# Optimization experiments

Hardware: AMD Instinct MI355X
Metric: run time of the kernel (lower is better)

Reference implementation:

```python
import jax, jax.numpy as jnp
import numpy as np

V, D, F, H, NB, S, B = 16384, 512, 2048, 8, 4, 512, 2
T_STEPS = 3      # config.T: number of PC inference iterations
GAMMA = 0.1      # state-update step size


def _layernorm(x, s, b):
    m = x.mean(-1, keepdims=True)
    v = ((x - m) ** 2).mean(-1, keepdims=True)
    return (x - m) * jax.lax.rsqrt(v + 1e-5) * s + b


def setup_inputs() -> dict:
    key = jax.random.key(0)
    ks = jax.random.split(key, 12)
    r = lambda k, sh: jax.random.normal(k, sh, jnp.float32) * 0.02
    return {
        'word_emb': r(ks[0], (V, D)),
        'pos_emb': r(ks[1], (S, D)),
        'Wq': r(ks[2], (NB, D, D)),
        'Wk': r(ks[3], (NB, D, D)),
        'Wv': r(ks[4], (NB, D, D)),
        'bq': jnp.zeros((NB, D), jnp.float32),
        'bk': jnp.zeros((NB, D), jnp.float32),
        'bv': jnp.zeros((NB, D), jnp.float32),
        'Wo': r(ks[5], (NB, D, D)),
        'bo': jnp.zeros((NB, D), jnp.float32),
        'ln1_s': jnp.ones((NB, D), jnp.float32),
        'ln1_b': jnp.zeros((NB, D), jnp.float32),
        'ln2_s': jnp.ones((NB, D), jnp.float32),
        'ln2_b': jnp.zeros((NB, D), jnp.float32),
        'W1': r(ks[6], (NB, D, F)),
        'b1': jnp.zeros((NB, F), jnp.float32),
        'W2': r(ks[7], (NB, F, D)),
        'b2': jnp.zeros((NB, D), jnp.float32),
        'Wout': r(ks[8], (D, V)),
        'bout': jnp.zeros((V,), jnp.float32),
        'input_ids': jax.random.randint(ks[9], (B, S), 0, V),
        'target_ids': jax.random.randint(ks[10], (B, S), 0, V),
    }


def _forward(word_emb, pos_emb, Wq, Wk, Wv, bq, bk, bv, Wo, bo,
             ln1_s, ln1_b, ln2_s, ln2_b, W1, b1, W2, b2, Wout, bout,
             input_ids, target_ids):
    Bsz, Sl = input_ids.shape
    dh = D // H
    scale = 1.0 / float(np.sqrt(dh))
    ids = jnp.clip(input_ids, 0, V - 1)
    target = jax.nn.one_hot(jnp.clip(target_ids, 0, V - 1), V, dtype=word_emb.dtype)
    # bottom prediction: word + position embeddings
    mu_emb = word_emb[ids] + pos_emb[jnp.arange(Sl)][None]  # (B,S,D)
    causal = jnp.tril(jnp.ones((Sl, Sl), bool))
    neg = jnp.finfo(word_emb.dtype).min

    def attn(x, b):
        h = _layernorm(x, ln1_s[b], ln1_b[b])
        q = (h @ Wq[b] + bq[b]).reshape(Bsz, Sl, H, dh)
        k = (h @ Wk[b] + bk[b]).reshape(Bsz, Sl, H, dh)
        v = (h @ Wv[b] + bv[b]).reshape(Bsz, Sl, H, dh)
        sc = jnp.einsum('bqhd,bkhd->bhqk', q, k) * scale
        sc = jnp.where(causal, sc, neg)
        a = jax.nn.softmax(sc, axis=-1)
        return jnp.einsum('bhqk,bkhd->bqhd', a, v).reshape(Bsz, Sl, D)

    # generative functions g[l]: x_l -> mu_{l+1}; 4 PC layers per block
    # (pc_qkv->attn ctx, pc_output->Wo, pc_layer1->gelu(fc1), pc_layer2->fc2)
    gs = []
    for b in range(NB):
        gs.append(lambda x, b=b: attn(x, b))
        gs.append(lambda x, b=b: x @ Wo[b] + bo[b])
        gs.append(lambda x, b=b: jax.nn.gelu(_layernorm(x, ln2_s[b], ln2_b[b]) @ W1[b] + b1[b]))
        gs.append(lambda x, b=b: x @ W2[b] + b2[b])
    g_top = lambda x: x @ Wout + bout  # output pc layer -> logits mu

    # init_x: forward sweep sets each latent to its prediction
    xs = [mu_emb]
    for g in gs:
        xs.append(g(xs[-1]))
    L = len(gs)

    # T-step iterative PC inference: eps_l = x_l - mu_l, top clamped to target
    # x_l <- x_l + GAMMA * (J_{g_l}(x_l)^T eps_{l+1} - eps_l)
    for _ in range(T_STEPS):
        preds, vjps = [], []
        for l in range(L):
            mu, vj = jax.vjp(gs[l], xs[l])
            preds.append(mu)
            vjps.append(vj)
        logits, vj_top = jax.vjp(g_top, xs[L])
        eps = [xs[0] - mu_emb] + [xs[l + 1] - preds[l] for l in range(L)]
        eps_top = logits - target
        new_xs = []
        for l in range(L + 1):
            td = vjps[l](eps[l + 1])[0] if l < L else vj_top(eps_top)[0]
            new_xs.append(xs[l] + GAMMA * (td - eps[l]))
        xs = new_xs

    return g_top(xs[L])  # get_mu('linear_output')


def reference(word_emb, pos_emb, Wq, Wk, Wv, bq, bk, bv, Wo, bo,
              ln1_s, ln1_b, ln2_s, ln2_b, W1, b1, W2, b2, Wout, bout,
              input_ids, target_ids):
    return _forward(word_emb, pos_emb, Wq, Wk, Wv, bq, bk, bv, Wo, bo,
                    ln1_s, ln1_b, ln2_s, ln2_b, W1, b1, W2, b2, Wout, bout,
                    input_ids, target_ids)
```

## Files before the change

### kernel.cpp

```cpp
#include <hip/hip_runtime.h>
#include <hip/hip_bf16.h>
#include <math.h>

#define D_   512
#define F_   2048
#define V_   16384
#define H_   8
#define DH_  64
#define S_   512
#define B_   2
#define M_   1024
#define MD_  (M_ * D_)
#define MF_  (M_ * F_)
#define GAMMA_ 0.1f

typedef unsigned int u32;
typedef unsigned short u16;
typedef __attribute__((ext_vector_type(4))) float f32x4;
typedef __attribute__((ext_vector_type(8))) short s16x8;
typedef __attribute__((ext_vector_type(4))) u16 u16x4;
typedef __attribute__((ext_vector_type(8))) u16 u16x8;

__device__ __forceinline__ u16 f2b(float f) {
    __hip_bfloat16 h = __float2bfloat16(f);
    return *reinterpret_cast<u16*>(&h);
}
__device__ __forceinline__ u16x4 pack4(f32x4 v) {
    u16x4 o; o.x = f2b(v[0]); o.y = f2b(v[1]); o.z = f2b(v[2]); o.w = f2b(v[3]);
    return o;
}

__device__ __forceinline__ void gl_lds16(const void* g, void* l) {
    __builtin_amdgcn_global_load_lds((const __attribute__((address_space(1))) u32*)g,
                                     (__attribute__((address_space(3))) u32*)l, 16, 0, 0);
}

__device__ __forceinline__ float gelu_f(float v) {
    float u = 0.7978845608028654f * (v + 0.044715f * v * v * v);
    return 0.5f * v * (1.f + tanhf(u));
}

__device__ __forceinline__ f32x4 xpose4(f32x4 v, int b) {
#pragma unroll
    for (int s = 1; s < 4; s <<= 1) {
        f32x4 nv;
#pragma unroll
        for (int j = 0; j < 4; ++j) {
            float ex = __shfl_xor(v[j ^ s], s, 64);
            nv[j] = ((b ^ j) & s) ? ex : v[j];
        }
        v = nv;
    }
    return v;
}

__device__ __forceinline__ float blk_sum(float v, float* sh) {
#pragma unroll
    for (int o = 32; o > 0; o >>= 1) v += __shfl_down(v, o, 64);
    int lane = threadIdx.x & 63, w = threadIdx.x >> 6;
    if (lane == 0) sh[w] = v;
    __syncthreads();
    float r = sh[0] + sh[1] + sh[2] + sh[3];
    __syncthreads();
    return r;
}

__device__ __forceinline__ float wave_sum(float v) {
#pragma unroll
    for (int o = 32; o > 0; o >>= 1) v += __shfl_xor(v, o, 64);
    return v;
}

#define E_F32   0
#define E_GELU  1
#define E_TD    2
#define E_X15B  3
#define E_EC    4
#define E_QKV3  5
#define E_OUT   6

template<int BK>
__device__ __forceinline__ int swz(int c, int row) {
    if constexpr (BK == 32) return c ^ ((row >> 1) & 3);
    else                    return c ^ (row & 7);
}

template<int BM, int BN, int BK, int FM, int FN, int EPI>
__global__ __launch_bounds__(256)
void mfma_gemm(const u16* __restrict__ A, const u16* __restrict__ B,
               float* __restrict__ Cf, u16* __restrict__ Cb,
               u16* __restrict__ Cb2, u16* __restrict__ Cb3,
               const float* __restrict__ bias,
               int K, int lda, int ldb, int ldc,
               long sC, long sKz, float alpha,
               const float* __restrict__ base, const float* __restrict__ subv,
               const float* __restrict__ cvec, const float* __restrict__ woutF,
               const int* __restrict__ tcl,
               float* __restrict__ ebF, u16* __restrict__ ebB)
{
    constexpr int WC = BN / (FN * 16);
    static_assert((BM / (FM * 16)) * WC == 4, "4 waves");
    constexpr int LPR = BK / 8;
    constexpr int RPI = 2048 / BK;
    __shared__ __align__(16) u16 Asl[2][BM * BK];
    __shared__ __align__(16) u16 Bsl[2][BN * BK];
    const int t = threadIdx.x, l = t & 63, wid = t >> 6;
    const int m0 = blockIdx.y * BM, n0 = blockIdx.x * BN;
    const long z = blockIdx.z;
    A += z * sKz;
    B += z * sKz;
    if (Cf) Cf += z * sC;

    f32x4 acc[FM][FN] = {};
    const int rm = (wid / WC) * (FM * 16), cn = (wid % WC) * (FN * 16);
    const int lr = l & 15, hi = l >> 4;
    const int srl = t / LPR, sc = t % LPR;

    auto stage = [&](int k0, int pb) {
#pragma unroll
        for (int i = 0; i < BM / RPI; ++i) {
            int row = i * RPI + srl;
            gl_lds16(A + (size_t)(m0 + row) * lda + k0 + swz<BK>(sc, row) * 8,
                     &Asl[pb][i * 2048 + t * 8]);
        }
#pragma unroll
        for (int i = 0; i < BN / RPI; ++i) {
            int row = i * RPI + srl;
            gl_lds16(B + (size_t)(n0 + row) * ldb + k0 + swz<BK>(sc, row) * 8,
                     &Bsl[pb][i * 2048 + t * 8]);
        }
    };
    auto compute = [&](int pb) {
#pragma unroll
        for (int kk = 0; kk < BK / 32; ++kk) {
            s16x8 av[FM], bv[FN];
#pragma unroll
            for (int fm = 0; fm < FM; ++fm)
                av[fm] = *(const s16x8*)&Asl[pb][(rm + fm * 16 + lr) * BK + swz<BK>(kk * 4 + hi, lr) * 8];
#pragma unroll
            for (int fn = 0; fn < FN; ++fn)
                bv[fn] = *(const s16x8*)&Bsl[pb][(cn + fn * 16 + lr) * BK + swz<BK>(kk * 4 + hi, lr) * 8];
#pragma unroll
            for (int fm = 0; fm < FM; ++fm)
#pragma unroll
                for (int fn = 0; fn < FN; ++fn)
                    acc[fm][fn] = __builtin_amdgcn_mfma_f32_16x16x32_bf16(av[fm], bv[fn], acc[fm][fn], 0, 0, 0);
        }
    };

    stage(0, 0);
    __syncthreads();
    int cur = 0;
    for (int k0 = BK; k0 < K; k0 += BK) {
        stage(k0, cur ^ 1);
        compute(cur);
        __syncthreads();
        cur ^= 1;
    }
    compute(cur);

    const int qb = lr & 3, qi = lr >> 2;
#pragma unroll
    for (int fm = 0; fm < FM; ++fm)
#pragma unroll
        for (int fn = 0; fn < FN; ++fn) {
            const int gm = m0 + rm + fm * 16 + hi * 4 + qb;
            const int gn0 = n0 + cn + fn * 16 + qi * 4;
            const size_t idx0 = (size_t)gm * ldc + gn0;
            if constexpr (EPI == E_QKV3) {
                const int gnf = n0 + cn + fn * 16;
                const int sel = gnf >> 9;
                if (sel < 2) {
                    f32x4 v = xpose4(acc[fm][fn], qb);
                    f32x4 bv4 = *(const f32x4*)&bias[gn0];
#pragma unroll
                    for (int j = 0; j < 4; ++j) v[j] += bv4[j];
                    int b = gm >> 9, s = gm & (S_ - 1);
                    int d9 = gn0 & 511, h = d9 >> 6, d = d9 & 63;
                    u16* dst = (sel == 0) ? Cb : Cb2;
                    *(u16x4*)&dst[(((size_t)(b * H_ + h) * S_ + s) << 6) + d] = pack4(v);
                } else {
                    const int gnl = gnf + lr;
                    const int gm0 = m0 + rm + fm * 16 + hi * 4;
                    int b = gm0 >> 9, s0 = gm0 & (S_ - 1);
                    int d9 = gnl & 511, h = d9 >> 6, d = d9 & 63;
                    float bb = bias[gnl];
                    f32x4 v = acc[fm][fn];
#pragma unroll
                    for (int j = 0; j < 4; ++j) v[j] += bb;
                    *(u16x4*)&Cb3[((((size_t)(b * H_ + h)) << 6) + d) * S_ + s0] = pack4(v);
                }
            } else {
                f32x4 v = xpose4(acc[fm][fn], qb);
                if constexpr (EPI == E_F32) {
#pragma unroll
                    for (int j = 0; j < 4; ++j) v[j] *= alpha;
                    if (bias) {
                        f32x4 bv4 = *(const f32x4*)&bias[gn0];
#pragma unroll
                        for (int j = 0; j < 4; ++j) v[j] += bv4[j];
                    }
                    *(f32x4*)&Cf[idx0] = v;
                    if (Cb) *(u16x4*)&Cb[idx0] = pack4(v);
                } else if constexpr (EPI == E_OUT) {
                    f32x4 bv4 = *(const f32x4*)&bias[gn0];
#pragma unroll
                    for (int j = 0; j < 4; ++j) v[j] += bv4[j];
                    *(f32x4*)&Cf[idx0] = v;
                } else if constexpr (EPI == E_GELU) {
                    f32x4 bv4 = *(const f32x4*)&bias[gn0];
#pragma unroll
                    for (int j = 0; j < 4; ++j) v[j] = gelu_f(v[j] + bv4[j]);
                    if (Cf) *(f32x4*)&Cf[idx0] = v;
                    *(u16x4*)&Cb[idx0] = pack4(v);
                } else if constexpr (EPI == E_TD) {
                    const int tc = tcl[gm];
                    f32x4 cv4 = *(const f32x4*)&cvec[gn0];
                    f32x4 ba4 = *(const f32x4*)&base[idx0];
                    f32x4 dlt, o2;
#pragma unroll
                    for (int j = 0; j < 4; ++j) {
                        float d = v[j] + cv4[j] - woutF[(size_t)(gn0 + j) * V_ + tc];
                        dlt[j] = GAMMA_ * d;
                    }
                    if (subv) {
                        f32x4 sv4 = *(const f32x4*)&subv[idx0];
#pragma unroll
                        for (int j = 0; j < 4; ++j) dlt[j] -= GAMMA_ * sv4[j];
                    }
#pragma unroll
                    for (int j = 0; j < 4; ++j) o2[j] = ba4[j] + dlt[j];
                    if (Cf) *(f32x4*)&Cf[idx0] = o2;
                    *(u16x4*)&Cb[idx0] = pack4(o2);
                    if (ebF) *(f32x4*)&ebF[idx0] = dlt;
                    if (ebB) *(u16x4*)&ebB[idx0] = pack4(dlt);
                } else if constexpr (EPI == E_X15B) {
                    f32x4 ba4 = *(const f32x4*)&base[idx0];
#pragma unroll
                    for (int j = 0; j < 4; ++j) v[j] = ba4[j] + GAMMA_ * v[j];
                    *(u16x4*)&Cb[idx0] = pack4(v);
                } else if constexpr (EPI == E_EC) {
                    f32x4 ba4 = *(const f32x4*)&base[idx0];
                    f32x4 bv4 = *(const f32x4*)&bias[gn0];
#pragma unroll
                    for (int j = 0; j < 4; ++j) v[j] = ba4[j] - (v[j] + bv4[j]);
                    *(f32x4*)&Cf[idx0] = v;
                }
            }
        }
}

__global__ __launch_bounds__(256)
void flash_attn(const u16* __restrict__ q, const u16* __restrict__ k,
                const u16* __restrict__ vT, u16* __restrict__ ctx)
{
    __shared__ __align__(16) u16 Ks[2][64 * 64];
    __shared__ __align__(16) u16 Vs[2][64 * 64];
    __shared__ __align__(16) u16 Ps[4][16 * 64];
    const int t = threadIdx.x, l = t & 63, w = t >> 6;
    const int qt = blockIdx.x, z = blockIdx.y;
    const int bb = z >> 3, hh = z & 7;
    const int lr = l & 15, hi = l >> 4;
    const u16* qp = q + (((size_t)z * S_ + qt * 64 + w * 16) << 6);
    const u16* kp = k + ((size_t)z * S_ << 6);
    const u16* vp = vT + (((size_t)z) << 6) * S_;

    const s16x8 aq0 = *(const s16x8*)&qp[lr * 64 + hi * 8];
    const s16x8 aq1 = *(const s16x8*)&qp[lr * 64 + 32 + hi * 8];

    f32x4 o[4] = {};
    float m[4], ls[4];
#pragma unroll
    for (int r = 0; r < 4; ++r) { m[r] = -3.0e38f; ls[r] = 0.f; }
    const int qrow = qt * 64 + w * 16 + hi * 4;
    const int srow = t >> 3, scl = t & 7;
    const int cg1 = (scl ^ (srow & 7)) * 8;
    const int srow2 = srow + 32;
    const int cg2 = (scl ^ (srow2 & 7)) * 8;
    const int sw7 = (lr & 7);

    auto stage = [&](int j, int pb) {
        gl_lds16(kp + ((size_t)(j * 64 + srow) << 6) + cg1, &Ks[pb][t * 8]);
        gl_lds16(vp + (size_t)srow * S_ + j * 64 + cg1, &Vs[pb][t * 8]);
        gl_lds16(kp + ((size_t)(j * 64 + srow2) << 6) + cg2, &Ks[pb][(t + 256) * 8]);
        gl_lds16(vp + (size_t)srow2 * S_ + j * 64 + cg2, &Vs[pb][(t + 256) * 8]);
    };

    stage(0, 0);
    __syncthreads();
    int cur = 0;
    for (int j = 0; j <= qt; ++j) {
        if (j < qt) stage(j + 1, cur ^ 1);

        float pv[4][4];
#pragma unroll
        for (int fn = 0; fn < 4; ++fn) {
            f32x4 acc = {};
            acc = __builtin_amdgcn_mfma_f32_16x16x32_bf16(aq0,
                    *(const s16x8*)&Ks[cur][((fn * 16 + lr) << 6) + ((hi ^ sw7) * 8)], acc, 0, 0, 0);
            acc = __builtin_amdgcn_mfma_f32_16x16x32_bf16(aq1,
                    *(const s16x8*)&Ks[cur][((fn * 16 + lr) << 6) + (((hi + 4) ^ sw7) * 8)], acc, 0, 0, 0);
#pragma unroll
            for (int r = 0; r < 4; ++r) pv[fn][r] = acc[r] * 0.125f;
        }
        if (j == qt) {
#pragma unroll
            for (int fn = 0; fn < 4; ++fn) {
                int col = j * 64 + fn * 16 + lr;
#pragma unroll
                for (int r = 0; r < 4; ++r)
                    if (col > qrow + r) pv[fn][r] = -3.0e38f;
            }
        }
        float sc[4], rs[4];
#pragma unroll
        for (int r = 0; r < 4; ++r) {
            float x = fmaxf(fmaxf(pv[0][r], pv[1][r]), fmaxf(pv[2][r], pv[3][r]));
#pragma unroll
            for (int off = 1; off < 16; off <<= 1) x = fmaxf(x, __shfl_xor(x, off, 64));
            float nm = fmaxf(m[r], x);
            sc[r] = expf(m[r] - nm);
            m[r] = nm;
            rs[r] = 0.f;
        }
#pragma unroll
        for (int fn = 0; fn < 4; ++fn)
#pragma unroll
            for (int r = 0; r < 4; ++r) {
                float p = expf(pv[fn][r] - m[r]);
                pv[fn][r] = p;
                rs[r] += p;
            }
#pragma unroll
        for (int r = 0; r < 4; ++r) {
#pragma unroll
            for (int off = 1; off < 16; off <<= 1) rs[r] += __shfl_xor(rs[r], off, 64);
            ls[r] = ls[r] * sc[r] + rs[r];
        }
#pragma unroll
        for (int fn = 0; fn < 4; ++fn)
#pragma unroll
            for (int r = 0; r < 4; ++r) o[fn][r] *= sc[r];
#pragma unroll
        for (int fn = 0; fn < 4; ++fn)
#pragma unroll
            for (int r = 0; r < 4; ++r) {
                int qr = hi * 4 + r;
                int ci = (2 * fn + (lr >> 3)) ^ (qr & 7);
                Ps[w][qr * 64 + ci * 8 + (lr & 7)] = f2b(pv[fn][r]);
            }
#pragma unroll
        for (int ks = 0; ks < 2; ++ks) {
            const s16x8 pa = *(const s16x8*)&Ps[w][lr * 64 + (((4 * ks + hi) ^ sw7) * 8)];
#pragma unroll
            for (int fn = 0; fn < 4; ++fn)
                o[fn] = __builtin_amdgcn_mfma_f32_16x16x32_bf16(pa,
                        *(const s16x8*)&Vs[cur][((fn * 16 + lr) << 6) + (((hi + 4 * ks) ^ sw7) * 8)], o[fn], 0, 0, 0);
        }
        __syncthreads();
        cur ^= 1;
    }
    float inv[4];
#pragma unroll
    for (int r = 0; r < 4; ++r) inv[r] = 1.f / ls[r];
    u16* cp = ctx + ((size_t)(bb * S_ + qt * 64 + w * 16) * D_) + hh * 64;
    const int qb = lr & 3, qi = lr >> 2;
#pragma unroll
    for (int fn = 0; fn < 4; ++fn) {
        f32x4 v = o[fn];
#pragma unroll
        for (int r = 0; r < 4; ++r) v[r] *= inv[r];
        v = xpose4(v, qb);
        *(u16x4*)&cp[(size_t)(hi * 4 + qb) * D_ + fn * 16 + qi * 4] = pack4(v);
    }
}

__global__ __launch_bounds__(256)
void mega_prep(const float* __restrict__ Wq, const float* __restrict__ Wk,
               const float* __restrict__ Wv, const float* __restrict__ Wo,
               const float* __restrict__ W1, const float* __restrict__ W2,
               const float* __restrict__ Wout,
               const float* __restrict__ bq, const float* __restrict__ bk,
               const float* __restrict__ bv, const int* __restrict__ target_ids,
               u16* __restrict__ wqkvT, u16* __restrict__ woT, u16* __restrict__ w1T,
               u16* __restrict__ w2T, u16* __restrict__ w2d, u16* __restrict__ woutT,
               u16* __restrict__ woutD, float* __restrict__ qkvb, int* __restrict__ tcl)
{
    __shared__ float tile[64][65];
    const int g = blockIdx.x, t = threadIdx.x;

    const float* in = nullptr;
    u16 *outT = nullptr, *outC = nullptr;
    int R = 512, C = 512, tx = 0, ty = 0;

    if (g < 768) {
        int sel = g / 256, rem = g % 256, zz = rem >> 6, tl = rem & 63;
        in = (sel == 0 ? Wq : sel == 1 ? Wk : Wv) + (size_t)zz * 262144;
        outT = wqkvT + (size_t)zz * 786432 + sel * 262144;
        tx = tl & 7; ty = tl >> 3;
    } else if (g < 1024) {
        int rem = g - 768, zz = rem >> 6, tl = rem & 63;
        in = Wo + (size_t)zz * 262144; outT = woT + (size_t)zz * 262144;
        tx = tl & 7; ty = tl >> 3;
    } else if (g < 2048) {
        int rem = g - 1024, zz = rem >> 8, tl = rem & 255;
        in = W1 + (size_t)zz * 1048576; outT = w1T + (size_t)zz * 1048576;
        C = 2048; tx = tl & 31; ty = tl >> 5;
    } else if (g < 3072) {
        int rem = g - 2048, zz = rem >> 8, tl = rem & 255;
        in = W2 + (size_t)zz * 1048576; outT = w2T + (size_t)zz * 1048576;
        if (zz == 3) outC = w2d;
        R = 2048; tx = tl & 7; ty = tl >> 3;
    } else if (g < 5120) {
        int tl = g - 3072;
        in = Wout; outT = woutT; outC = woutD;
        C = 16384; tx = tl & 255; ty = tl >> 8;
    } else {
        for (int i = t; i < M_; i += 256) {
            int v = target_ids[i];
            tcl[i] = v < 0 ? 0 : (v > V_ - 1 ? V_ - 1 : v);
        }
        for (int i = t; i < 4 * 1536; i += 256) {
            int b = i / 1536, j = i - b * 1536;
            qkvb[i] = (j < 512) ? bq[b * 512 + j]
                    : (j < 1024) ? bk[b * 512 + j - 512] : bv[b * 512 + j - 1024];
        }
        return;
    }

    const int r0 = ty * 64, c0 = tx * 64;
#pragma unroll
    for (int p = 0; p < 4; ++p) {
        int row = p * 16 + (t >> 4), col = (t & 15) * 4;
        float4 v = *(const float4*)&in[(size_t)(r0 + row) * C + c0 + col];
        tile[row][col] = v.x; tile[row][col + 1] = v.y;
        tile[row][col + 2] = v.z; tile[row][col + 3] = v.w;
        if (outC) {
            f32x4 fv; fv[0] = v.x; fv[1] = v.y; fv[2] = v.z; fv[3] = v.w;
            *(u16x4*)&outC[(size_t)(r0 + row) * C + c0 + col] = pack4(fv);
        }
    }
    __syncthreads();
#pragma unroll
    for (int p = 0; p < 2; ++p) {
        int orow = p * 32 + (t >> 3), oc = (t & 7) * 8;
        u16x8 o;
#pragma unroll
        for (int j = 0; j < 8; ++j) o[j] = f2b(tile[oc + j][orow]);
        *(u16x8*)&outT[(size_t)(c0 + orow) * R + r0 + oc] = o;
    }
}

__global__ __launch_bounds__(256)
void cvec_kernel(const float* __restrict__ Wout, const float* __restrict__ bout,
                 float* __restrict__ c)
{
    __shared__ float sh[4];
    int d = blockIdx.x;
    const float* row = Wout + (size_t)d * V_;
    float s = 0.f;
    for (int v = threadIdx.x * 4; v < V_; v += 1024) {
        float4 a = *(const float4*)&row[v];
        float4 b = *(const float4*)&bout[v];
        s += a.x * b.x + a.y * b.y + a.z * b.z + a.w * b.w;
    }
    float r = blk_sum(s, sh);
    if (threadIdx.x == 0) c[d] = r;
}

__global__ void gred_kernel(const float* __restrict__ P, u16* __restrict__ G)
{
    int i = blockIdx.x * blockDim.x + threadIdx.x;
    if (i < D_ * D_) {
        float s = 0.f;
#pragma unroll
        for (int zz = 0; zz < 16; ++zz) s += P[(size_t)zz * D_ * D_ + i];
        G[i] = f2b(s);
    }
}

__global__ void embed_kernel(const float4* __restrict__ we, const float4* __restrict__ pe,
                             const int* __restrict__ ids, float4* __restrict__ o)
{
    int t = blockIdx.x * blockDim.x + threadIdx.x;
    int d4 = t & 127, row = t >> 7;
    int ss = row & (S_ - 1);
    int id = ids[row];
    id = id < 0 ? 0 : (id > V_ - 1 ? V_ - 1 : id);
    float4 a = we[(size_t)id * 128 + d4];
    float4 b = pe[(size_t)ss * 128 + d4];
    o[(size_t)row * 128 + d4] = make_float4(a.x + b.x, a.y + b.y, a.z + b.z, a.w + b.w);
}

__global__ __launch_bounds__(256)
void ln_fwd_kernel(const float* __restrict__ x, const float* __restrict__ s,
                   const float* __restrict__ bb, u16* __restrict__ h)
{
    const int l = threadIdx.x & 63, w = threadIdx.x >> 6;
    const int row = blockIdx.x * 4 + w;
    const float* xr = x + (size_t)row * D_;
    const int c0 = l * 8;
    float4 a = *(const float4*)&xr[c0];
    float4 b = *(const float4*)&xr[c0 + 4];
    float sum = a.x + a.y + a.z + a.w + b.x + b.y + b.z + b.w;
    float mu = wave_sum(sum) * (1.f / D_);
    float d0 = a.x - mu, d1 = a.y - mu, d2 = a.z - mu, d3 = a.w - mu;
    float d4 = b.x - mu, d5 = b.y - mu, d6 = b.z - mu, d7 = b.w - mu;
    float vs = d0*d0 + d1*d1 + d2*d2 + d3*d3 + d4*d4 + d5*d5 + d6*d6 + d7*d7;
    float var = wave_sum(vs) * (1.f / D_);
    float r = rsqrtf(var + 1e-5f);
    float4 s0 = *(const float4*)&s[c0], s1 = *(const float4*)&s[c0 + 4];
    float4 b0 = *(const float4*)&bb[c0], b1 = *(const float4*)&bb[c0 + 4];
    u16* hr = h + (size_t)row * D_;
    f32x4 o0, o1;
    o0[0] = d0 * r * s0.x + b0.x; o0[1] = d1 * r * s0.y + b0.y;
    o0[2] = d2 * r * s0.z + b0.z; o0[3] = d3 * r * s0.w + b0.w;
    o1[0] = d4 * r * s1.x + b1.x; o1[1] = d5 * r * s1.y + b1.y;
    o1[2] = d6 * r * s1.z + b1.z; o1[3] = d7 * r * s1.w + b1.w;
    *(u16x4*)&hr[c0] = pack4(o0);
    *(u16x4*)&hr[c0 + 4] = pack4(o1);
}

extern "C" void kernel_launch(void* const* d_in, const int* in_sizes, int n_in,
                              void* d_out, int out_size, void* d_ws, size_t ws_size,
                              hipStream_t stream)
{
    (void)in_sizes; (void)n_in; (void)out_size;
    const float* Wq  = (const float*)d_in[2];
    const float* Wk  = (const float*)d_in[3];
    const float* Wv  = (const float*)d_in[4];
    const float* bq  = (const float*)d_in[5];
    const float* bk  = (const float*)d_in[6];
    const float* bv  = (const float*)d_in[7];
    const float* Wo  = (const float*)d_in[8];
    const float* bo  = (const float*)d_in[9];
    const float* ln1_s = (const float*)d_in[10];
    const float* ln1_b = (const float*)d_in[11];
    const float* ln2_s = (const float*)d_in[12];
    const float* ln2_b = (const float*)d_in[13];
    const float* W1  = (const float*)d_in[14];
    const float* b1  = (const float*)d_in[15];
    const float* W2  = (const float*)d_in[16];
    const float* b2  = (const float*)d_in[17];
    const float* Wout = (const float*)d_in[18];
    const float* bout = (const float*)d_in[19];
    const int* input_ids  = (const int*)d_in[20];
    const int* target_ids = (const int*)d_in[21];
    float* out = (float*)d_out;

    char* wsb = (char*)d_ws;
    size_t off = 0;
    auto alloc = [&](size_t bytes) -> void* {
        off = (off + 255) & ~(size_t)255;
        void* p = wsb + off; off += bytes; return p;
    };
    u16* wqkvT = (u16*)alloc((size_t)4 * 1536 * D_ * 2);
    u16* woT   = (u16*)alloc((size_t)4 * D_ * D_ * 2);
    u16* w1T   = (u16*)alloc((size_t)4 * D_ * F_ * 2);
    u16* w2T   = (u16*)alloc((size_t)4 * D_ * F_ * 2);
    u16* w2d   = (u16*)alloc((size_t)F_ * D_ * 2);
    u16* woutT = (u16*)alloc((size_t)V_ * D_ * 2);
    u16* G_b   = (u16*)alloc((size_t)D_ * D_ * 2);
    float* qkvb = (float*)alloc((size_t)4 * 1536 * 4);
    float* bufA = (float*)alloc((size_t)MF_ * 4);
    float* bufB = (float*)alloc((size_t)MD_ * 4);
    u16* h_b    = (u16*)alloc((size_t)MD_ * 2);
    u16* gelu_b = (u16*)alloc((size_t)MF_ * 2);
    u16* x16_b  = (u16*)alloc((size_t)MD_ * 2);
    float* cvec = (float*)alloc(D_ * 4);
    int* tcl    = (int*)alloc(M_ * 4);
    size_t uStart = (off + 255) & ~(size_t)255;
    off = uStart;
    u16* woutD   = (u16*)alloc((size_t)V_ * D_ * 2);
    float* Gpart = (float*)alloc((size_t)16 * D_ * D_ * 4);
    size_t endG = off;
    off = uStart;
    u16* q_b   = (u16*)alloc((size_t)MD_ * 2);
    u16* k_b   = (u16*)alloc((size_t)MD_ * 2);
    u16* v_b   = (u16*)alloc((size_t)MD_ * 2);
    u16* ctx_b = (u16*)alloc((size_t)MD_ * 2);
    size_t endA = off;
    off = uStart;
    float* xA  = (float*)alloc((size_t)MD_ * 4);
    float* xB  = (float*)alloc((size_t)MD_ * 4);
    float* eb  = (float*)alloc((size_t)MD_ * 4);
    float* ec  = (float*)alloc((size_t)MD_ * 4);
    u16* xA_b  = (u16*)alloc((size_t)MD_ * 2);
    u16* xB_b  = (u16*)alloc((size_t)MD_ * 2);
    u16* xC_b  = (u16*)alloc((size_t)MD_ * 2);
    u16* eb_b  = (u16*)alloc((size_t)MD_ * 2);
    u16* x15b_b = (u16*)alloc((size_t)MF_ * 2);
    size_t endT = off;
    size_t need = endG > endA ? endG : endA;
    if (endT > need) need = endT;
    if (need > ws_size) return;

    dim3 blk(256);
    const long NL = 0;
    #define GZ nullptr, nullptr, nullptr, nullptr, nullptr, nullptr, nullptr

    mega_prep<<<dim3(5121), blk, 0, stream>>>(Wq, Wk, Wv, Wo, W1, W2, Wout,
        bq, bk, bv, target_ids, wqkvT, woT, w1T, w2T, w2d, woutT, woutD, qkvb, tcl);
    cvec_kernel<<<dim3(D_), blk, 0, stream>>>(Wout, bout, cvec);
    mfma_gemm<128, 128, 64, 4, 4, E_F32><<<dim3(4, 4, 16), blk, 0, stream>>>(
        woutD, woutD, Gpart, nullptr, nullptr, nullptr, nullptr, 1024, V_, V_, D_,
        (long)D_ * D_, 1024, 1.f, GZ);
    gred_kernel<<<dim3(1024), blk, 0, stream>>>(Gpart, G_b);

    embed_kernel<<<dim3(512), blk, 0, stream>>>((const float4*)d_in[0], (const float4*)d_in[1],
                                                input_ids, (float4*)bufB);
    for (int b = 0; b < 4; ++b) {
        const size_t wDD = (size_t)b * D_ * D_, wDF = (size_t)b * D_ * F_;
        ln_fwd_kernel<<<dim3(M_ / 4), blk, 0, stream>>>(bufB, ln1_s + b * D_, ln1_b + b * D_, h_b);
        mfma_gemm<128, 64, 64, 4, 2, E_QKV3><<<dim3(24, 8, 1), blk, 0, stream>>>(
            h_b, wqkvT + (size_t)b * 1536 * 512, nullptr, q_b, k_b, v_b,
            qkvb + b * 1536, D_, D_, D_, 0, NL, NL, 1.f, GZ);
        flash_attn<<<dim3(8, 16), blk, 0, stream>>>(q_b, k_b, v_b, ctx_b);
        mfma_gemm<64, 64, 128, 2, 2, E_F32><<<dim3(8, 16, 1), blk, 0, stream>>>(
            ctx_b, woT + wDD, bufB, nullptr, nullptr, nullptr, bo + b * D_,
            D_, D_, D_, D_, NL, NL, 1.f, GZ);
        ln_fwd_kernel<<<dim3(M_ / 4), blk, 0, stream>>>(bufB, ln2_s + b * D_, ln2_b + b * D_, h_b);
        mfma_gemm<64, 64, 128, 2, 2, E_GELU><<<dim3(32, 16, 1), blk, 0, stream>>>(
            h_b, w1T + wDF, (b == 3) ? bufA : nullptr, gelu_b, nullptr, nullptr, b1 + b * F_,
            D_, D_, D_, F_, NL, NL, 1.f, GZ);
        mfma_gemm<64, 64, 128, 2, 2, E_F32><<<dim3(8, 16, 1), blk, 0, stream>>>(
            gelu_b, w2T + wDF, bufB, (b == 3) ? x16_b : nullptr, nullptr, nullptr, b2 + b * D_,
            F_, F_, F_, D_, NL, NL, 1.f, GZ);
    }

    mfma_gemm<64, 64, 128, 2, 2, E_TD><<<dim3(8, 16, 1), blk, 0, stream>>>(
        x16_b, G_b, xA, xA_b, nullptr, nullptr, nullptr, D_, D_, D_, D_, NL, NL, 1.f,
        bufB, nullptr, cvec, Wout, tcl, eb, eb_b);
    mfma_gemm<64, 64, 128, 2, 2, E_TD><<<dim3(8, 16, 1), blk, 0, stream>>>(
        xA_b, G_b, xB, xB_b, nullptr, nullptr, nullptr, D_, D_, D_, D_, NL, NL, 1.f,
        xA, eb, cvec, Wout, tcl, nullptr, nullptr);
    mfma_gemm<64, 64, 128, 2, 2, E_X15B><<<dim3(32, 16, 1), blk, 0, stream>>>(
        eb_b, w2d, nullptr, x15b_b, nullptr, nullptr, nullptr, D_, D_, D_, F_, NL, NL, 1.f,
        bufA, nullptr, nullptr, nullptr, nullptr, nullptr, nullptr);
    mfma_gemm<64, 64, 128, 2, 2, E_EC><<<dim3(8, 16, 1), blk, 0, stream>>>(
        x15b_b, w2T + (size_t)3 * D_ * F_, ec, nullptr, nullptr, nullptr, b2 + 3 * D_,
        F_, F_, F_, D_, NL, NL, 1.f,
        xB, nullptr, nullptr, nullptr, nullptr, nullptr, nullptr);
    mfma_gemm<64, 64, 128, 2, 2, E_TD><<<dim3(8, 16, 1), blk, 0, stream>>>(
        xB_b, G_b, nullptr, xC_b, nullptr, nullptr, nullptr, D_, D_, D_, D_, NL, NL, 1.f,
        xB, ec, cvec, Wout, tcl, nullptr, nullptr);
    mfma_gemm<128, 256, 32, 4, 8, E_OUT><<<dim3(64, 8, 1), blk, 0, stream>>>(
        xC_b, woutT, out, nullptr, nullptr, nullptr, bout, D_, D_, D_, V_, NL, NL, 1.f, GZ);
    #undef GZ
}
```

Baseline: 450.0 us.

## Precompute W2^T W2 Gram, fuse cvec into transpose prep, gather bf16 Wout rows

Replaces the two-step W2-based error correction (a D×F GEMM producing an intermediate then an F×D GEMM) with a single D×D GEMM against a precomputed H2 = W2·W2ᵀ, so the intermediate layer-15 state is never materialised. The cvec reduction is folded into the Wout transpose pass via atomics, prep work for bias/target clamps moves to a small separate kernel, and the TD epilogue gathers contiguous bf16 rows of transposed Wout instead of strided fp32 reads. It also drops the fp32 GELU output store and raises BK for the QKV and output GEMMs. The algebraic shortcut and bf16 Wout gather change rounding, and the atomic cvec sum makes that result order-dependent.

Measured after the change: 435.1 us. 1.03x faster.

```diff
diff --git a/kernel.cpp b/kernel.cpp
--- a/kernel.cpp
+++ b/kernel.cpp
@@ -25,6 +25,10 @@
     __hip_bfloat16 h = __float2bfloat16(f);
     return *reinterpret_cast<u16*>(&h);
 }
+__device__ __forceinline__ float b2f(u16 v) {
+    u32 u = ((u32)v) << 16;
+    float f; __builtin_memcpy(&f, &u, 4); return f;
+}
 __device__ __forceinline__ u16x4 pack4(f32x4 v) {
     u16x4 o; o.x = f2b(v[0]); o.y = f2b(v[1]); o.z = f2b(v[2]); o.w = f2b(v[3]);
     return o;
@@ -54,17 +58,6 @@
     return v;
 }
 
-__device__ __forceinline__ float blk_sum(float v, float* sh) {
-#pragma unroll
-    for (int o = 32; o > 0; o >>= 1) v += __shfl_down(v, o, 64);
-    int lane = threadIdx.x & 63, w = threadIdx.x >> 6;
-    if (lane == 0) sh[w] = v;
-    __syncthreads();
-    float r = sh[0] + sh[1] + sh[2] + sh[3];
-    __syncthreads();
-    return r;
-}
-
 __device__ __forceinline__ float wave_sum(float v) {
 #pragma unroll
     for (int o = 32; o > 0; o >>= 1) v += __shfl_xor(v, o, 64);
@@ -74,10 +67,10 @@
 #define E_F32   0
 #define E_GELU  1
 #define E_TD    2
-#define E_X15B  3
-#define E_EC    4
-#define E_QKV3  5
-#define E_OUT   6
+#define E_EC2   3
+#define E_QKV3  4
+#define E_OUT   5
+#define E_BF16  6
 
 template<int BK>
 __device__ __forceinline__ int swz(int c, int row) {
@@ -94,7 +87,7 @@
                int K, int lda, int ldb, int ldc,
                long sC, long sKz, float alpha,
                const float* __restrict__ base, const float* __restrict__ subv,
-               const float* __restrict__ cvec, const float* __restrict__ woutF,
+               const float* __restrict__ cvec, const u16* __restrict__ woutTb,
                const int* __restrict__ tcl,
                float* __restrict__ ebF, u16* __restrict__ ebB)
 {
@@ -211,18 +204,16 @@
                     f32x4 bv4 = *(const f32x4*)&bias[gn0];
 #pragma unroll
                     for (int j = 0; j < 4; ++j) v[j] = gelu_f(v[j] + bv4[j]);
-                    if (Cf) *(f32x4*)&Cf[idx0] = v;
                     *(u16x4*)&Cb[idx0] = pack4(v);
                 } else if constexpr (EPI == E_TD) {
                     const int tc = tcl[gm];
                     f32x4 cv4 = *(const f32x4*)&cvec[gn0];
                     f32x4 ba4 = *(const f32x4*)&base[idx0];
+                    u16x4 gv = *(const u16x4*)&woutTb[(size_t)tc * D_ + gn0];
                     f32x4 dlt, o2;
 #pragma unroll
-                    for (int j = 0; j < 4; ++j) {
-                        float d = v[j] + cv4[j] - woutF[(size_t)(gn0 + j) * V_ + tc];
-                        dlt[j] = GAMMA_ * d;
-                    }
+                    for (int j = 0; j < 4; ++j)
+                        dlt[j] = GAMMA_ * (v[j] + cv4[j] - b2f(gv[j]));
                     if (subv) {
                         f32x4 sv4 = *(const f32x4*)&subv[idx0];
 #pragma unroll
@@ -234,17 +225,14 @@
                     *(u16x4*)&Cb[idx0] = pack4(o2);
                     if (ebF) *(f32x4*)&ebF[idx0] = dlt;
                     if (ebB) *(u16x4*)&ebB[idx0] = pack4(dlt);
-                } else if constexpr (EPI == E_X15B) {
+                } else if constexpr (EPI == E_EC2) {
                     f32x4 ba4 = *(const f32x4*)&base[idx0];
-#pragma unroll
-                    for (int j = 0; j < 4; ++j) v[j] = ba4[j] + GAMMA_ * v[j];
+                    f32x4 sv4 = *(const f32x4*)&subv[idx0];
+#pragma unroll
+                    for (int j = 0; j < 4; ++j) v[j] = ba4[j] - sv4[j] - GAMMA_ * v[j];
+                    *(f32x4*)&Cf[idx0] = v;
+                } else if constexpr (EPI == E_BF16) {
                     *(u16x4*)&Cb[idx0] = pack4(v);
-                } else if constexpr (EPI == E_EC) {
-                    f32x4 ba4 = *(const f32x4*)&base[idx0];
-                    f32x4 bv4 = *(const f32x4*)&bias[gn0];
-#pragma unroll
-                    for (int j = 0; j < 4; ++j) v[j] = ba4[j] - (v[j] + bv4[j]);
-                    *(f32x4*)&Cf[idx0] = v;
                 }
             }
         }
@@ -376,15 +364,32 @@
 }
 
 __global__ __launch_bounds__(256)
+void prep0(const float* __restrict__ bq, const float* __restrict__ bk,
+           const float* __restrict__ bv, const int* __restrict__ target_ids,
+           float* __restrict__ qkvb, int* __restrict__ tcl, float* __restrict__ cvec)
+{
+    int i = blockIdx.x * 256 + threadIdx.x;
+    if (i < 512) cvec[i] = 0.f;
+    else if (i < 1536) {
+        int mm = i - 512;
+        int v = target_ids[mm];
+        tcl[mm] = v < 0 ? 0 : (v > V_ - 1 ? V_ - 1 : v);
+    } else if (i < 1536 + 6144) {
+        int j = i - 1536;
+        int b = j / 1536, r = j - b * 1536;
+        qkvb[j] = (r < 512) ? bq[b * 512 + r]
+                : (r < 1024) ? bk[b * 512 + r - 512] : bv[b * 512 + r - 1024];
+    }
+}
+
+__global__ __launch_bounds__(256)
 void mega_prep(const float* __restrict__ Wq, const float* __restrict__ Wk,
                const float* __restrict__ Wv, const float* __restrict__ Wo,
                const float* __restrict__ W1, const float* __restrict__ W2,
-               const float* __restrict__ Wout,
-               const float* __restrict__ bq, const float* __restrict__ bk,
-               const float* __restrict__ bv, const int* __restrict__ target_ids,
+               const float* __restrict__ Wout, const float* __restrict__ bout,
                u16* __restrict__ wqkvT, u16* __restrict__ woT, u16* __restrict__ w1T,
-               u16* __restrict__ w2T, u16* __restrict__ w2d, u16* __restrict__ woutT,
-               u16* __restrict__ woutD, float* __restrict__ qkvb, int* __restrict__ tcl)
+               u16* __restrict__ w2T, u16* __restrict__ woutT,
+               u16* __restrict__ woutD, float* __restrict__ cvec)
 {
     __shared__ float tile[64][65];
     const int g = blockIdx.x, t = threadIdx.x;
@@ -392,6 +397,7 @@
     const float* in = nullptr;
     u16 *outT = nullptr, *outC = nullptr;
     int R = 512, C = 512, tx = 0, ty = 0;
+    bool doCvec = false;
 
     if (g < 768) {
         int sel = g / 256, rem = g % 256, zz = rem >> 6, tl = rem & 63;
@@ -409,23 +415,11 @@
     } else if (g < 3072) {
         int rem = g - 2048, zz = rem >> 8, tl = rem & 255;
         in = W2 + (size_t)zz * 1048576; outT = w2T + (size_t)zz * 1048576;
-        if (zz == 3) outC = w2d;
         R = 2048; tx = tl & 7; ty = tl >> 3;
-    } else if (g < 5120) {
+    } else {
         int tl = g - 3072;
-        in = Wout; outT = woutT; outC = woutD;
+        in = Wout; outT = woutT; outC = woutD; doCvec = true;
         C = 16384; tx = tl & 255; ty = tl >> 8;
-    } else {
-        for (int i = t; i < M_; i += 256) {
-            int v = target_ids[i];
-            tcl[i] = v < 0 ? 0 : (v > V_ - 1 ? V_ - 1 : v);
-        }
-        for (int i = t; i < 4 * 1536; i += 256) {
-            int b = i / 1536, j = i - b * 1536;
-            qkvb[i] = (j < 512) ? bq[b * 512 + j]
-                    : (j < 1024) ? bk[b * 512 + j - 512] : bv[b * 512 + j - 1024];
-        }
-        return;
     }
 
     const int r0 = ty * 64, c0 = tx * 64;
@@ -449,23 +443,16 @@
         for (int j = 0; j < 8; ++j) o[j] = f2b(tile[oc + j][orow]);
         *(u16x8*)&outT[(size_t)(c0 + orow) * R + r0 + oc] = o;
     }
-}
-
-__global__ __launch_bounds__(256)
-void cvec_kernel(const float* __restrict__ Wout, const float* __restrict__ bout,
-                 float* __restrict__ c)
-{
-    __shared__ float sh[4];
-    int d = blockIdx.x;
-    const float* row = Wout + (size_t)d * V_;
-    float s = 0.f;
-    for (int v = threadIdx.x * 4; v < V_; v += 1024) {
-        float4 a = *(const float4*)&row[v];
-        float4 b = *(const float4*)&bout[v];
-        s += a.x * b.x + a.y * b.y + a.z * b.z + a.w * b.w;
-    }
-    float r = blk_sum(s, sh);
-    if (threadIdx.x == 0) c[d] = r;
+    if (doCvec) {
+        int r = t >> 2, q = t & 3;
+        float s = 0.f;
+#pragma unroll
+        for (int i = 0; i < 16; ++i)
+            s += tile[r][q * 16 + i] * bout[c0 + q * 16 + i];
+        s += __shfl_xor(s, 1, 64);
+        s += __shfl_xor(s, 2, 64);
+        if (q == 0) atomicAdd(&cvec[r0 + r], s);
+    }
 }
 
 __global__ void gred_kernel(const float* __restrict__ P, u16* __restrict__ G)
@@ -558,11 +545,10 @@
     u16* woT   = (u16*)alloc((size_t)4 * D_ * D_ * 2);
     u16* w1T   = (u16*)alloc((size_t)4 * D_ * F_ * 2);
     u16* w2T   = (u16*)alloc((size_t)4 * D_ * F_ * 2);
-    u16* w2d   = (u16*)alloc((size_t)F_ * D_ * 2);
     u16* woutT = (u16*)alloc((size_t)V_ * D_ * 2);
     u16* G_b   = (u16*)alloc((size_t)D_ * D_ * 2);
+    u16* H2_b  = (u16*)alloc((size_t)D_ * D_ * 2);
     float* qkvb = (float*)alloc((size_t)4 * 1536 * 4);
-    float* bufA = (float*)alloc((size_t)MF_ * 4);
     float* bufB = (float*)alloc((size_t)MD_ * 4);
     u16* h_b    = (u16*)alloc((size_t)MD_ * 2);
     u16* gelu_b = (u16*)alloc((size_t)MF_ * 2);
@@ -589,7 +575,6 @@
     u16* xB_b  = (u16*)alloc((size_t)MD_ * 2);
     u16* xC_b  = (u16*)alloc((size_t)MD_ * 2);
     u16* eb_b  = (u16*)alloc((size_t)MD_ * 2);
-    u16* x15b_b = (u16*)alloc((size_t)MF_ * 2);
     size_t endT = off;
     size_t need = endG > endA ? endG : endA;
     if (endT > need) need = endT;
@@ -599,20 +584,23 @@
     const long NL = 0;
     #define GZ nullptr, nullptr, nullptr, nullptr, nullptr, nullptr, nullptr
 
-    mega_prep<<<dim3(5121), blk, 0, stream>>>(Wq, Wk, Wv, Wo, W1, W2, Wout,
-        bq, bk, bv, target_ids, wqkvT, woT, w1T, w2T, w2d, woutT, woutD, qkvb, tcl);
-    cvec_kernel<<<dim3(D_), blk, 0, stream>>>(Wout, bout, cvec);
+    prep0<<<dim3(32), blk, 0, stream>>>(bq, bk, bv, target_ids, qkvb, tcl, cvec);
+    mega_prep<<<dim3(5120), blk, 0, stream>>>(Wq, Wk, Wv, Wo, W1, W2, Wout, bout,
+        wqkvT, woT, w1T, w2T, woutT, woutD, cvec);
     mfma_gemm<128, 128, 64, 4, 4, E_F32><<<dim3(4, 4, 16), blk, 0, stream>>>(
         woutD, woutD, Gpart, nullptr, nullptr, nullptr, nullptr, 1024, V_, V_, D_,
         (long)D_ * D_, 1024, 1.f, GZ);
     gred_kernel<<<dim3(1024), blk, 0, stream>>>(Gpart, G_b);
+    mfma_gemm<64, 64, 128, 2, 2, E_BF16><<<dim3(8, 8, 1), blk, 0, stream>>>(
+        w2T + (size_t)3 * D_ * F_, w2T + (size_t)3 * D_ * F_, nullptr, H2_b,
+        nullptr, nullptr, nullptr, F_, F_, F_, D_, NL, NL, 1.f, GZ);
 
     embed_kernel<<<dim3(512), blk, 0, stream>>>((const float4*)d_in[0], (const float4*)d_in[1],
                                                 input_ids, (float4*)bufB);
     for (int b = 0; b < 4; ++b) {
         const size_t wDD = (size_t)b * D_ * D_, wDF = (size_t)b * D_ * F_;
         ln_fwd_kernel<<<dim3(M_ / 4), blk, 0, stream>>>(bufB, ln1_s + b * D_, ln1_b + b * D_, h_b);
-        mfma_gemm<128, 64, 64, 4, 2, E_QKV3><<<dim3(24, 8, 1), blk, 0, stream>>>(
+        mfma_gemm<128, 64, 128, 4, 2, E_QKV3><<<dim3(24, 8, 1), blk, 0, stream>>>(
             h_b, wqkvT + (size_t)b * 1536 * 512, nullptr, q_b, k_b, v_b,
             qkvb + b * 1536, D_, D_, D_, 0, NL, NL, 1.f, GZ);
         flash_attn<<<dim3(8, 16), blk, 0, stream>>>(q_b, k_b, v_b, ctx_b);
@@ -621,7 +609,7 @@
             D_, D_, D_, D_, NL, NL, 1.f, GZ);
         ln_fwd_kernel<<<dim3(M_ / 4), blk, 0, stream>>>(bufB, ln2_s + b * D_, ln2_b + b * D_, h_b);
         mfma_gemm<64, 64, 128, 2, 2, E_GELU><<<dim3(32, 16, 1), blk, 0, stream>>>(
-            h_b, w1T + wDF, (b == 3) ? bufA : nullptr, gelu_b, nullptr, nullptr, b1 + b * F_,
+            h_b, w1T + wDF, nullptr, gelu_b, nullptr, nullptr, b1 + b * F_,
             D_, D_, D_, F_, NL, NL, 1.f, GZ);
         mfma_gemm<64, 64, 128, 2, 2, E_F32><<<dim3(8, 16, 1), blk, 0, stream>>>(
             gelu_b, w2T + wDF, bufB, (b == 3) ? x16_b : nullptr, nullptr, nullptr, b2 + b * D_,
@@ -630,21 +618,17 @@
 
     mfma_gemm<64, 64, 128, 2, 2, E_TD><<<dim3(8, 16, 1), blk, 0, stream>>>(
         x16_b, G_b, xA, xA_b, nullptr, nullptr, nullptr, D_, D_, D_, D_, NL, NL, 1.f,
-        bufB, nullptr, cvec, Wout, tcl, eb, eb_b);
+        bufB, nullptr, cvec, woutT, tcl, eb, eb_b);
     mfma_gemm<64, 64, 128, 2, 2, E_TD><<<dim3(8, 16, 1), blk, 0, stream>>>(
         xA_b, G_b, xB, xB_b, nullptr, nullptr, nullptr, D_, D_, D_, D_, NL, NL, 1.f,
-        xA, eb, cvec, Wout, tcl, nullptr, nullptr);
-    mfma_gemm<64, 64, 128, 2, 2, E_X15B><<<dim3(32, 16, 1), blk, 0, stream>>>(
-        eb_b, w2d, nullptr, x15b_b, nullptr, nullptr, nullptr, D_, D_, D_, F_, NL, NL, 1.f,
-        bufA, nullptr, nullptr, nullptr, nullptr, nullptr, nullptr);
-    mfma_gemm<64, 64, 128, 2, 2, E_EC><<<dim3(8, 16, 1), blk, 0, stream>>>(
-        x15b_b, w2T + (size_t)3 * D_ * F_, ec, nullptr, nullptr, nullptr, b2 + 3 * D_,
-        F_, F_, F_, D_, NL, NL, 1.f,
-        xB, nullptr, nullptr, nullptr, nullptr, nullptr, nullptr);
+        xA, eb, cvec, woutT, tcl, nullptr, nullptr);
+    mfma_gemm<64, 64, 128, 2, 2, E_EC2><<<dim3(8, 16, 1), blk, 0, stream>>>(
+        eb_b, H2_b, ec, nullptr, nullptr, nullptr, nullptr, D_, D_, D_, D_, NL, NL, 1.f,
+        xB, bufB, nullptr, nullptr, nullptr, nullptr, nullptr);
     mfma_gemm<64, 64, 128, 2, 2, E_TD><<<dim3(8, 16, 1), blk, 0, stream>>>(
         xB_b, G_b, nullptr, xC_b, nullptr, nullptr, nullptr, D_, D_, D_, D_, NL, NL, 1.f,
-        xB, ec, cvec, Wout, tcl, nullptr, nullptr);
-    mfma_gemm<128, 256, 32, 4, 8, E_OUT><<<dim3(64, 8, 1), blk, 0, stream>>>(
+        xB, ec, cvec, woutT, tcl, nullptr, nullptr);
+    mfma_gemm<128, 256, 64, 4, 8, E_OUT><<<dim3(64, 8, 1), blk, 0, stream>>>(
         xC_b, woutT, out, nullptr, nullptr, nullptr, bout, D_, D_, D_, V_, NL, NL, 1.f, GZ);
     #undef GZ
 }
```
